# Kernel optimization log

Hardware: AMD Instinct MI355X
Metric: run time of the kernel (lower is better)

## Reference

```python
import jax, jax.numpy as jnp
import numpy as np

B, NA, NE = 1024, 15, 16
N_AGENTS = NA + 1
BN = B * N_AGENTS
D_OWN = D_ALL = D_EN = 32
H, NH, NMOVE, RD = 256, 4, 6, 8
HD = H // NH
GATE = 1.0
NEG = -1e9  # stand-in for -inf (safe under autodiff)


def _gelu(x):
    return jax.nn.gelu(x, approximate=False)  # torch nn.GELU default is exact


def _ln(x, g, b, eps=1e-5):
    m = x.mean(-1, keepdims=True)
    v = ((x - m) ** 2).mean(-1, keepdims=True)
    return (x - m) * jax.lax.rsqrt(v + eps) * g + b


def _masked_mean(x, mask, axis):
    w = mask[..., None].astype(x.dtype)
    return (x * w).sum(axis) / jnp.clip(w.sum(axis), 1e-8)


def _mha(q, kv, mask, Wq, Wk, Wv, Wo):
    # q: [BN,H], kv: [BN,M,H], mask: [BN,M] bool
    bn = q.shape[0]
    qh = (q @ Wq.T).reshape(bn, NH, HD)
    kh = (kv @ Wk.T).reshape(bn, -1, NH, HD)
    vh = (kv @ Wv.T).reshape(bn, -1, NH, HD)
    scores = jnp.einsum('bhd,bmhd->bhm', qh, kh) / np.sqrt(HD)
    scores = jnp.where(mask[:, None, :], scores, NEG)
    attn = jax.nn.softmax(scores, axis=-1)
    ctx = jnp.einsum('bhm,bmhd->bhd', attn, vh).reshape(bn, H)
    return ctx @ Wo.T


def setup_inputs() -> dict:
    key = jax.random.key(0)
    ks = iter(jax.random.split(key, 64))
    nrm = lambda *s: jax.random.normal(next(ks), s, dtype=jnp.float32)
    w = lambda o, i: nrm(o, i) * 0.02
    inp = dict(
        bs=B,
        own_feats=nrm(BN, 1, D_OWN),
        ally_feats=nrm(BN, NA, D_ALL),
        enemy_feats=nrm(BN, NE, D_EN),
        hidden_state=nrm(B, N_AGENTS, H),
        own_W=w(H, D_OWN), own_b=jnp.zeros(H),
        ally_W=w(H, D_ALL), ally_b=jnp.zeros(H),
        en_W=w(H, D_EN), en_b=jnp.zeros(H),
        aA_Wq=w(H, H), aA_Wk=w(H, H), aA_Wv=w(H, H), aA_Wo=w(H, H),
        aE_Wq=w(H, H), aE_Wk=w(H, H), aE_Wv=w(H, H), aE_Wo=w(H, H),
        fuse_W1=w(H, 3 * H), fuse_b1=jnp.zeros(H), fuse_g1=jnp.ones(H), fuse_be1=jnp.zeros(H),
        fuse_W2=w(H, H), fuse_b2=jnp.zeros(H),
        pool_W1=w(128, 3 * H), pool_b1=jnp.zeros(128), pool_g1=jnp.ones(128), pool_be1=jnp.zeros(128),
        pool_W2=w(128, 128), pool_b2=jnp.zeros(128),
        role_W1=w(128, 128), role_b1=jnp.zeros(128), role_g1=jnp.ones(128), role_be1=jnp.zeros(128),
        role_W2=w(RD, 128), role_b2=jnp.zeros(RD),
        rln_g=jnp.ones(RD), rln_b=jnp.zeros(RD),
        gru_Wih=w(3 * H, H + RD), gru_Whh=w(3 * H, H),
        gru_bih=jnp.zeros(3 * H), gru_bhh=jnp.zeros(3 * H),
        qn_W=w(NMOVE, H), qn_b=jnp.zeros(NMOVE),
        qp_W=w(H, H + RD), kp_W=w(H, H),
    )
    return inp


def reference(bs, own_feats, ally_feats, enemy_feats, hidden_state,
              own_W, own_b, ally_W, ally_b, en_W, en_b,
              aA_Wq, aA_Wk, aA_Wv, aA_Wo, aE_Wq, aE_Wk, aE_Wv, aE_Wo,
              fuse_W1, fuse_b1, fuse_g1, fuse_be1, fuse_W2, fuse_b2,
              pool_W1, pool_b1, pool_g1, pool_be1, pool_W2, pool_b2,
              role_W1, role_b1, role_g1, role_be1, role_W2, role_b2,
              rln_g, rln_b, gru_Wih, gru_Whh, gru_bih, gru_bhh,
              qn_W, qn_b, qp_W, kp_W):
    ally_mask = ~jnp.all(ally_feats == 0, axis=-1)   # [BN,Na]
    enemy_mask = ~jnp.all(enemy_feats == 0, axis=-1)  # [BN,Ne]

    own_e = own_feats @ own_W.T + own_b        # [BN,1,H]
    ally_e = ally_feats @ ally_W.T + ally_b    # [BN,Na,H]
    enemy_e = enemy_feats @ en_W.T + en_b      # [BN,Ne,H]
    self_emb = own_e[:, 0]                     # [BN,H]

    cA = _mha(self_emb, ally_e, ally_mask, aA_Wq, aA_Wk, aA_Wv, aA_Wo)
    cE = _mha(self_emb, enemy_e, enemy_mask, aE_Wq, aE_Wk, aE_Wv, aE_Wo)

    # fuse MLP: Linear -> GELU -> LN -> Linear
    f_in = jnp.concatenate([self_emb, cA, cE], axis=-1)
    h0 = _ln(_gelu(f_in @ fuse_W1.T + fuse_b1), fuse_g1, fuse_be1) @ fuse_W2.T + fuse_b2

    pA = _masked_mean(ally_e, ally_mask, 1)
    pE = _masked_mean(enemy_e, enemy_mask, 1)
    p_in = jnp.concatenate([self_emb, pA, pE], axis=-1)
    pooled = _ln(_gelu(p_in @ pool_W1.T + pool_b1), pool_g1, pool_be1) @ pool_W2.T + pool_b2
    r = jnp.tanh(_ln(_gelu(pooled @ role_W1.T + role_b1), role_g1, role_be1) @ role_W2.T + role_b2)
    r = _ln(r, rln_g, rln_b)

    # GRUCell (torch convention)
    h_prev = hidden_state.reshape(-1, H)
    x = jnp.concatenate([h0, GATE * r], axis=-1)
    gi = x @ gru_Wih.T + gru_bih
    gh = h_prev @ gru_Whh.T + gru_bhh
    i_r, i_z, i_n = jnp.split(gi, 3, axis=-1)
    h_r, h_z, h_n = jnp.split(gh, 3, axis=-1)
    rg = jax.nn.sigmoid(i_r + h_r)
    zg = jax.nn.sigmoid(i_z + h_z)
    ng = jnp.tanh(i_n + rg * h_n)
    h_cur = (1.0 - zg) * ng + zg * h_prev

    q_normal = h_cur @ qn_W.T + qn_b  # [BN,n_move]

    q_vec = jnp.concatenate([h_cur, GATE * r], axis=-1) @ qp_W.T  # [BN,H]
    k_vec = enemy_e @ kp_W.T                                       # [BN,Ne,H]
    logits = jnp.einsum('bj,bmj->bm', q_vec, k_vec) / np.sqrt(H)
    logits = jnp.where(enemy_mask, logits, NEG)
    denom = jnp.clip(enemy_mask.sum(-1, keepdims=True), 1).astype(logits.dtype)
    mean_valid = jnp.where(enemy_mask, logits, 0.0).sum(-1, keepdims=True) / denom
    q_interact = logits - mean_valid

    Q = jnp.concatenate([q_normal, q_interact], axis=-1)
    h_out = h_cur.reshape(bs, N_AGENTS, H)
    return Q, h_out
```

## Files before the change

### kernel.cpp

```cpp
#include <hip/hip_runtime.h>
#include <hip/hip_bf16.h>


#define MROWS 16384

typedef __attribute__((ext_vector_type(8))) short short8;
typedef __attribute__((ext_vector_type(4))) float float4v;
typedef __attribute__((ext_vector_type(4))) unsigned short ushort4v;
typedef __attribute__((ext_vector_type(2))) unsigned short ushort2v;

__device__ __forceinline__ unsigned short f2b(float f) {
    __hip_bfloat16 h = __float2bfloat16(f);
    return *reinterpret_cast<unsigned short*>(&h);
}
__device__ __forceinline__ float b2f(unsigned short u) {
    __hip_bfloat16 h;
    *reinterpret_cast<unsigned short*>(&h) = u;
    return __bfloat162float(h);
}
__device__ __forceinline__ void gll16(const unsigned short* g, unsigned short* l) {
    __builtin_amdgcn_global_load_lds((const __attribute__((address_space(1))) void*)g,
                                     (__attribute__((address_space(3))) void*)l, 16, 0, 0);
}

__global__ void cvt_misc(const float* __restrict__ hidden, const float* __restrict__ ownf,
                         unsigned short* __restrict__ XG, unsigned short* __restrict__ OWNb,
                         unsigned short* __restrict__ zbuf) {
    int idx = blockIdx.x * 256 + threadIdx.x;
    const int nh = MROWS * 64;
    const int no = MROWS * 8;
    if (idx < nh) {
        int row = idx >> 6, c4 = (idx & 63) * 4;
        float4 v = *(const float4*)(hidden + (size_t)row * 256 + c4);
        ushort4v d = { f2b(v.x), f2b(v.y), f2b(v.z), f2b(v.w) };
        *(ushort4v*)(XG + (size_t)row * 520 + 264 + c4) = d;
    } else if (idx < nh + no) {
        int j = idx - nh;
        int row = j >> 3, c4 = (j & 7) * 4;
        float4 v = *(const float4*)(ownf + (size_t)row * 32 + c4);
        ushort4v d = { f2b(v.x), f2b(v.y), f2b(v.z), f2b(v.w) };
        *(ushort4v*)(OWNb + (size_t)row * 32 + c4) = d;
    } else if (idx < nh + no + 16) {
        int j = idx - nh - no;
        ((uint4*)zbuf)[j] = make_uint4(0u, 0u, 0u, 0u);
    }
}

struct TOp {
    int type;
    const float* A; int sAi, sAk;
    const float* B; int sBj, sBk;
    void* O; int sOi;
    int I, J, K;
    int nb; int aB, bB, oB;
};
struct TOpSet { int n; int tiles[26]; TOp ops[26]; };

__global__ __launch_bounds__(256)
void compose_tiled(TOpSet S) {
    int t = blockIdx.x;
    int op = 0;
    while (op < S.n && t >= S.tiles[op]) { t -= S.tiles[op]; op++; }
    if (op >= S.n) return;
    TOp o = S.ops[op];
    int ti = (o.I + 31) >> 5, tj = (o.J + 31) >> 5;
    int per = ti * tj;
    int b = t / per;
    int rem = t - b * per;
    int i0 = (rem / tj) * 32, j0 = (rem % tj) * 32;
    int tid = threadIdx.x;
    if (o.type >= 2) {
        for (int e = tid; e < 1024; e += 256) {
            int r = e >> 5, c = e & 31;
            int i = i0 + r, j = j0 + c;
            if (i < o.I && j < o.J) {
                unsigned short v = 0;
                if (o.type == 2) v = f2b(o.A[(long)b * o.aB + (long)i * o.sAi + (long)j * o.sAk]);
                ((unsigned short*)o.O)[(long)b * o.oB + (long)i * o.sOi + j] = v;
            }
        }
        return;
    }
    __shared__ float As[32][33];
    __shared__ float Bs[32][33];
    int tx = tid & 15, ty = tid >> 4;
    float a00 = 0.f, a01 = 0.f, a10 = 0.f, a11 = 0.f;
    const float* Ab = o.A + (long)b * o.aB;
    const float* Bb = o.B + (long)b * o.bB;
    for (int k0 = 0; k0 < o.K; k0 += 32) {
        for (int e = tid; e < 1024; e += 256) {
            int r = e >> 5, c = e & 31;
            As[r][c] = (i0 + r < o.I && k0 + c < o.K)
                       ? Ab[(long)(i0 + r) * o.sAi + (long)(k0 + c) * o.sAk] : 0.f;
            Bs[r][c] = (k0 + r < o.K && j0 + c < o.J)
                       ? Bb[(long)(j0 + c) * o.sBj + (long)(k0 + r) * o.sBk] : 0.f;
        }
        __syncthreads();
#pragma unroll
        for (int k = 0; k < 32; k++) {
            float x0 = As[ty * 2][k], x1 = As[ty * 2 + 1][k];
            float y0 = Bs[k][tx * 2], y1 = Bs[k][tx * 2 + 1];
            a00 += x0 * y0; a01 += x0 * y1; a10 += x1 * y0; a11 += x1 * y1;
        }
        __syncthreads();
    }
    int i = i0 + ty * 2, j = j0 + tx * 2;
    float vals[2][2] = {{a00, a01}, {a10, a11}};
#pragma unroll
    for (int di = 0; di < 2; di++)
#pragma unroll
        for (int dj = 0; dj < 2; dj++) {
            int ii = i + di, jj = j + dj;
            if (ii < o.I && jj < o.J) {
                long oidx = (long)b * o.oB + (long)ii * o.sOi + jj;
                if (o.type == 0) ((unsigned short*)o.O)[oidx] = f2b(vals[di][dj]);
                else ((float*)o.O)[oidx] = vals[di][dj];
            }
        }
}

struct MOp { const float* A; int sAi; const float* x; const float* b1; const float* b2; float* out; int I, K; };
struct MOpSet { int n; int waves[10]; MOp ops[10]; };

__global__ void mv_ops(MOpSet S) {
    int wid = blockIdx.x * 4 + (threadIdx.x >> 6);
    int lane = threadIdx.x & 63;
    int op = 0;
    while (op < S.n && wid >= S.waves[op]) { wid -= S.waves[op]; op++; }
    if (op >= S.n) return;
    MOp o = S.ops[op];
    float s = 0.f;
    for (int k = lane; k < o.K; k += 64) s += o.A[(long)wid * o.sAi + k] * o.x[k];
    for (int off = 32; off; off >>= 1) s += __shfl_xor(s, off, 64);
    if (lane == 0) {
        if (o.b1) s += o.b1[wid];
        if (o.b2) s += o.b2[wid];
        o.out[wid] = s;
    }
}

template<int BM, int BN>
__global__ __launch_bounds__(256, 4)
void gemm_bf16(const unsigned short* __restrict__ A, int lda,
               const unsigned short* __restrict__ W,
               const float* __restrict__ bias,
               unsigned short* __restrict__ C, int ldc,
               int N, int K, int act,
               const unsigned short* __restrict__ zbuf) {
    constexpr int MI = BM / 32, NJ = BN / 32;
    __shared__ __align__(16) unsigned short As[2][BM * 32];
    __shared__ __align__(16) unsigned short Bs[2][BN * 32];
    int tid = threadIdx.x;
    int m0 = blockIdx.x * BM, n0 = blockIdx.y * BN;
    int wave = tid >> 6, lane = tid & 63;
    int wm = (wave & 1) * (BM / 2), wn = (wave >> 1) * (BN / 2);
    int l16 = lane & 15, quad = lane >> 4;

    float4v acc[MI][NJ];
#pragma unroll
    for (int i = 0; i < MI; i++)
#pragma unroll
        for (int j = 0; j < NJ; j++) acc[i][j] = (float4v){0.f, 0.f, 0.f, 0.f};

    int swz = ((l16 >> 1) & 3) * 8;
    int nt = (K + 31) >> 5;

    auto stage = [&](int buf, int k0) {
#pragma unroll
        for (int s0 = 0; s0 < BM * 4; s0 += 256) {
            int s = s0 + tid;
            int row = s >> 2;
            int cg = (s & 3) ^ ((row >> 1) & 3);
            int ka = k0 + cg * 8;
            gll16((ka < K) ? A + (size_t)(m0 + row) * lda + ka : zbuf, &As[buf][s * 8]);
        }
#pragma unroll
        for (int s0 = 0; s0 < BN * 4; s0 += 256) {
            int s = s0 + tid;
            int row = s >> 2;
            int cg = (s & 3) ^ ((row >> 1) & 3);
            int ka = k0 + cg * 8;
            gll16((ka < K && n0 + row < N) ? W + (size_t)(n0 + row) * K + ka : zbuf,
                  &Bs[buf][s * 8]);
        }
    };
    auto compute = [&](int buf) {
        short8 a[MI], b[NJ];
#pragma unroll
        for (int i = 0; i < MI; i++)
            a[i] = *(const short8*)(&As[buf][(wm + i * 16 + l16) * 32 + ((quad * 8) ^ swz)]);
#pragma unroll
        for (int j = 0; j < NJ; j++)
            b[j] = *(const short8*)(&Bs[buf][(wn + j * 16 + l16) * 32 + ((quad * 8) ^ swz)]);
#pragma unroll
        for (int i = 0; i < MI; i++)
#pragma unroll
            for (int j = 0; j < NJ; j++)
                acc[i][j] = __builtin_amdgcn_mfma_f32_16x16x32_bf16(a[i], b[j], acc[i][j], 0, 0, 0);
    };

    stage(0, 0);
    asm volatile("s_waitcnt vmcnt(0)" ::: "memory");
    __builtin_amdgcn_s_barrier();
    for (int t = 0; t < nt - 1; t++) {
        stage((t + 1) & 1, (t + 1) << 5);
        compute(t & 1);
        asm volatile("s_waitcnt vmcnt(0)" ::: "memory");
        __builtin_amdgcn_s_barrier();
    }
    compute((nt - 1) & 1);

#pragma unroll
    for (int i = 0; i < MI; i++) {
#pragma unroll
        for (int j = 0; j < NJ; j++) {
#pragma unroll
            for (int rr = 0; rr < 4; rr++) {
                int rowm = m0 + wm + i * 16 + quad * 4 + rr;
                int coln = wn + j * 16 + l16;
                if (n0 + coln >= N) continue;
                float v = acc[i][j][rr];
                if (bias) v += bias[n0 + coln];
                if (act == 1) v = 0.5f * v * (1.f + erff(v * 0.70710678f));
                C[(size_t)rowm * ldc + n0 + coln] = f2b(v);
            }
        }
    }
}

__global__ __launch_bounds__(256)
void ln_fp(const unsigned short* __restrict__ FPC,
           const float* __restrict__ g1, const float* __restrict__ be1,
           const float* __restrict__ g2, const float* __restrict__ be2,
           unsigned short* __restrict__ XG, unsigned short* __restrict__ T2) {
    int tid = threadIdx.x;
    size_t row = (size_t)blockIdx.x * 4 + (tid >> 6);
    int l = tid & 63;
    const unsigned short* src = FPC + row * 384;
    ushort4v vf = *(const ushort4v*)(src + l * 4);
    ushort2v vp = *(const ushort2v*)(src + 256 + l * 2);
    float f0 = b2f(vf[0]), f1 = b2f(vf[1]), f2v = b2f(vf[2]), f3 = b2f(vf[3]);
    float p0 = b2f(vp[0]), p1 = b2f(vp[1]);
    float s = f0 + f1 + f2v + f3;
    float q = f0 * f0 + f1 * f1 + f2v * f2v + f3 * f3;
    float s2 = p0 + p1, q2 = p0 * p0 + p1 * p1;
    for (int o = 32; o; o >>= 1) {
        s += __shfl_xor(s, o, 64); q += __shfl_xor(q, o, 64);
        s2 += __shfl_xor(s2, o, 64); q2 += __shfl_xor(q2, o, 64);
    }
    float mean = s * (1.f / 256.f);
    float rstd = rsqrtf(q * (1.f / 256.f) - mean * mean + 1e-5f);
    float4 g = *(const float4*)(g1 + l * 4);
    float4 be = *(const float4*)(be1 + l * 4);
    ushort4v o4;
    o4[0] = f2b((f0 - mean) * rstd * g.x + be.x);
    o4[1] = f2b((f1 - mean) * rstd * g.y + be.y);
    o4[2] = f2b((f2v - mean) * rstd * g.z + be.z);
    o4[3] = f2b((f3 - mean) * rstd * g.w + be.w);
    *(ushort4v*)(XG + row * 520 + l * 4) = o4;
    float mean2 = s2 * (1.f / 128.f);
    float rstd2 = rsqrtf(q2 * (1.f / 128.f) - mean2 * mean2 + 1e-5f);
    float2 gg = *(const float2*)(g2 + l * 2);
    float2 bb = *(const float2*)(be2 + l * 2);
    ushort2v o2;
    o2[0] = f2b((p0 - mean2) * rstd2 * gg.x + bb.x);
    o2[1] = f2b((p1 - mean2) * rstd2 * gg.y + bb.y);
    *(ushort2v*)(T2 + row * 128 + l * 2) = o2;
}

__global__ __launch_bounds__(256)
void glue_attn(const float* __restrict__ allyf, const float* __restrict__ enemyf,
               const float* __restrict__ ownf, const unsigned short* __restrict__ QKS,
               unsigned short* __restrict__ X) {
    __shared__ __align__(16) float af[4][540];
    __shared__ __align__(16) float ef[4][576];
    __shared__ __align__(16) float qk[4][288];
    __shared__ float attnA[4][64];
    __shared__ float attnE[4][64];
    __shared__ float mskA[4][16];
    __shared__ float mskE[4][16];
    int tid = threadIdx.x;
    size_t rb = (size_t)blockIdx.x * 4;

    for (int idx = tid; idx < 480; idx += 256) {
        int r = idx / 120, ch = idx - r * 120;
        float4 v = *(const float4*)(allyf + ((rb + r) * 480 + ch * 4));
        *(float4*)&af[r][(ch >> 3) * 36 + (ch & 7) * 4] = v;
    }
    for (int idx = tid; idx < 512; idx += 256) {
        int r = idx >> 7, ch = idx & 127;
        float4 v = *(const float4*)(enemyf + ((rb + r) * 512 + ch * 4));
        *(float4*)&ef[r][(ch >> 3) * 36 + (ch & 7) * 4] = v;
    }
    if (tid < 128) {
        int r = tid >> 5, ch = tid & 31;
        short8 v = *(const short8*)(QKS + (rb + r) * 256 + ch * 8);
#pragma unroll
        for (int j = 0; j < 8; j++)
            qk[r][(ch >> 2) * 36 + (ch & 3) * 8 + j] = b2f((unsigned short)v[j]);
    } else {
        int r = (tid - 128) >> 5, c = (tid - 128) & 31;
        X[(rb + r) * 360 + c] = f2b(ownf[(rb + r) * 32 + c]);
    }
    if (tid < 24) {
        int r = tid / 6, c = 98 + tid % 6;
        X[(rb + r) * 360 + c] = 0;
    }
    __syncthreads();

    if (tid < 248) {
        int pair = tid >> 1, half = tid & 1;
        int r = pair / 31, e = pair - r * 31;
        const float* base = (e < 15) ? &af[r][e * 36] : &ef[r][(e - 15) * 36];
        const float4* b4 = (const float4*)base + half * 4;
        bool nz = false;
#pragma unroll
        for (int k = 0; k < 4; k++) {
            float4 v = b4[k];
            nz |= (v.x != 0.f) || (v.y != 0.f) || (v.z != 0.f) || (v.w != 0.f);
        }
        int other = __shfl_xor((int)nz, 1, 64);
        float mv = (nz || other != 0) ? 1.f : 0.f;
        if (half == 0) {
            if (e < 15) mskA[r][e] = mv; else mskE[r][e - 15] = mv;
        }
    } else if (tid < 252) {
        mskA[tid - 248][15] = 0.f;
    }
    __syncthreads();

    int r = tid >> 6, lane = tid & 63;
    int h = lane >> 4, m = lane & 15;
    {
        float sc = -3.0e38f;
        if (m < 15) {
            const float4* qa = (const float4*)&qk[r][h * 36];
            const float4* aa = (const float4*)&af[r][m * 36];
            float s = 0.f;
#pragma unroll
            for (int k = 0; k < 8; k++) {
                float4 q = qa[k], a = aa[k];
                s += q.x * a.x + q.y * a.y + q.z * a.z + q.w * a.w;
            }
            sc = (mskA[r][m] > 0.f) ? s * 0.125f : -1e9f;
        }
        float mx = sc;
        for (int o = 8; o; o >>= 1) mx = fmaxf(mx, __shfl_xor(mx, o, 64));
        float e = (m < 15) ? __expf(sc - mx) : 0.f;
        float sm = e;
        for (int o = 8; o; o >>= 1) sm += __shfl_xor(sm, o, 64);
        attnA[r][h * 16 + m] = e / sm;
    }
    {
        const float4* qa = (const float4*)&qk[r][(4 + h) * 36];
        const float4* aa = (const float4*)&ef[r][m * 36];
        float s = 0.f;
#pragma unroll
        for (int k = 0; k < 8; k++) {
            float4 q = qa[k], a = aa[k];
            s += q.x * a.x + q.y * a.y + q.z * a.z + q.w * a.w;
        }
        float sc = (mskE[r][m] > 0.f) ? s * 0.125f : -1e9f;
        float mx = sc;
        for (int o = 8; o; o >>= 1) mx = fmaxf(mx, __shfl_xor(mx, o, 64));
        float e = __expf(sc - mx);
        float sm = e;
        for (int o = 8; o; o >>= 1) sm += __shfl_xor(sm, o, 64);
        attnE[r][h * 16 + m] = e / sm;
    }
    __syncthreads();
    size_t row = rb + r;
#pragma unroll
    for (int it = 0; it < 2; it++) {
        int idx = lane + it * 64;
        int hh = idx >> 5, c = idx & 31;
        float sA = 0.f;
        for (int mm = 0; mm < 15; mm++) sA += attnA[r][hh * 16 + mm] * af[r][mm * 36 + c];
        X[row * 360 + 104 + idx] = f2b(sA);
        float sE = 0.f;
        for (int mm = 0; mm < 16; mm++) sE += attnE[r][hh * 16 + mm] * ef[r][mm * 36 + c];
        X[row * 360 + 232 + idx] = f2b(sE);
    }
    if (lane < 32) {
        float cnt = 0.f;
        for (int mm = 0; mm < 15; mm++) cnt += mskA[r][mm];
        float s = 0.f;
        for (int mm = 0; mm < 15; mm++) s += af[r][mm * 36 + lane];
        X[row * 360 + 32 + lane] = f2b(s / fmaxf(cnt, 1e-8f));
        if (lane == 0) X[row * 360 + 96] = f2b(cnt > 0.f ? 1.f : 0.f);
    } else {
        int c = lane - 32;
        float cnt = 0.f;
        for (int mm = 0; mm < 16; mm++) cnt += mskE[r][mm];
        float s = 0.f;
        for (int mm = 0; mm < 16; mm++) s += ef[r][mm * 36 + c];
        X[row * 360 + 64 + c] = f2b(s / fmaxf(cnt, 1e-8f));
        if (c == 0) X[row * 360 + 97] = f2b(cnt > 0.f ? 1.f : 0.f);
    }
}

__global__ __launch_bounds__(256)
void ln_role(const unsigned short* __restrict__ T3, const float* __restrict__ g1,
             const float* __restrict__ be1, const float* __restrict__ W2,
             const float* __restrict__ b2, const float* __restrict__ rg,
             const float* __restrict__ rb, unsigned short* __restrict__ XG) {
    __shared__ float t3[32][132];
    __shared__ float gl[128], bl[128];
    int tid = threadIdx.x;
    size_t base = (size_t)blockIdx.x * 4096;
    for (int idx = tid; idx < 4096; idx += 256)
        t3[idx >> 7][idx & 127] = b2f(T3[base + idx]);
    if (tid < 128) { gl[tid] = g1[tid]; bl[tid] = be1[tid]; }
    __syncthreads();
    int r = tid >> 3, t = tid & 7;
    float s = 0.f, q = 0.f;
    for (int c = 0; c < 16; c++) { float v = t3[r][t * 16 + c]; s += v; q += v * v; }
    for (int o = 4; o; o >>= 1) { s += __shfl_xor(s, o, 8); q += __shfl_xor(q, o, 8); }
    float mean = s * (1.f / 128.f);
    float var = q * (1.f / 128.f) - mean * mean;
    float rstd = rsqrtf(var + 1e-5f);
    float acc = b2[t];
    const float* w = W2 + t * 128;
    for (int d = 0; d < 128; d++)
        acc += w[d] * ((t3[r][d] - mean) * rstd * gl[d] + bl[d]);
    float v = tanhf(acc);
    float mn = v;
    for (int o = 4; o; o >>= 1) mn += __shfl_xor(mn, o, 8);
    mn *= 0.125f;
    float dv = v - mn, qq = dv * dv;
    for (int o = 4; o; o >>= 1) qq += __shfl_xor(qq, o, 8);
    qq *= 0.125f;
    size_t row = (size_t)blockIdx.x * 32 + r;
    XG[row * 520 + 256 + t] = f2b(dv * rsqrtf(qq + 1e-5f) * rg[t] + rb[t]);
}

__global__ __launch_bounds__(256)
void glue_gru(const unsigned short* __restrict__ G, const float* __restrict__ hp,
              float* __restrict__ hout, unsigned short* __restrict__ XQ,
              const unsigned short* __restrict__ XG) {
    int tid = threadIdx.x;
    size_t row = (size_t)blockIdx.x * 4 + (tid >> 6);
    int l = tid & 63;
    size_t b = row * 1024;
    ushort4v vr = *(const ushort4v*)(G + b + l * 4);
    ushort4v vz = *(const ushort4v*)(G + b + 256 + l * 4);
    ushort4v vi = *(const ushort4v*)(G + b + 512 + l * 4);
    ushort4v vh = *(const ushort4v*)(G + b + 768 + l * 4);
    float4 hv = *(const float4*)(hp + row * 256 + l * 4);
    float hpv[4] = {hv.x, hv.y, hv.z, hv.w};
    float hov[4];
    ushort4v xq;
#pragma unroll
    for (int j = 0; j < 4; j++) {
        float rg = 1.f / (1.f + __expf(-b2f(vr[j])));
        float zg = 1.f / (1.f + __expf(-b2f(vz[j])));
        float ng = tanhf(b2f(vi[j]) + rg * b2f(vh[j]));
        float h = (1.f - zg) * ng + zg * hpv[j];
        hov[j] = h;
        xq[j] = f2b(h);
    }
    *(float4*)(hout + row * 256 + l * 4) = make_float4(hov[0], hov[1], hov[2], hov[3]);
    *(ushort4v*)(XQ + row * 264 + l * 4) = xq;
    if (l < 2)
        ((ushort4v*)(XQ + row * 264 + 256))[l] = ((const ushort4v*)(XG + row * 520 + 256))[l];
}

__global__ __launch_bounds__(256)
void glue_final(const unsigned short* __restrict__ QWS, const float* __restrict__ efeats,
                const float* __restrict__ qnb, float* __restrict__ Q) {
    __shared__ __align__(16) float ef[8][576];
    __shared__ __align__(16) float qw[8][40];
    int tid = threadIdx.x;
    size_t rb = (size_t)blockIdx.x * 8;
    for (int idx = tid; idx < 1024; idx += 256) {
        int r = idx >> 7, ch = idx & 127;
        float4 v = *(const float4*)(efeats + (rb + r) * 512 + ch * 4);
        *(float4*)&ef[r][(ch >> 3) * 36 + (ch & 7) * 4] = v;
    }
    for (int idx = tid; idx < 320; idx += 256) {
        int r = idx / 40, c = idx % 40;
        qw[r][c] = b2f(QWS[(rb + r) * 40 + c]);
    }
    __syncthreads();
    int r = tid >> 5, t = tid & 31;
    size_t row = rb + r;
    float lg = 0.f, mk = 0.f;
    if (t < 16) {
        const float4* fr = (const float4*)&ef[r][t * 36];
        const float4* qv = (const float4*)&qw[r][0];
        bool nz = false;
        float s = 0.f;
#pragma unroll
        for (int k = 0; k < 8; k++) {
            float4 a = fr[k], b = qv[k];
            nz |= (a.x != 0.f) || (a.y != 0.f) || (a.z != 0.f) || (a.w != 0.f);
            s += a.x * b.x + a.y * b.y + a.z * b.z + a.w * b.w;
        }
        mk = nz ? 1.f : 0.f;
        lg = (s + qw[r][32]) * 0.0625f;
    }
    float sv = mk * lg, cv = mk;
    for (int o = 8; o; o >>= 1) { sv += __shfl_xor(sv, o, 64); cv += __shfl_xor(cv, o, 64); }
    float mean = sv / fmaxf(cv, 1.f);
    if (t < 16) Q[row * 22 + 6 + t] = (mk > 0.f ? lg : -1e9f) - mean;
    if (t < 6) Q[row * 22 + t] = qw[r][33 + t] + qnb[t];
}

extern "C" void kernel_launch(void* const* d_in, const int* in_sizes, int n_in,
                              void* d_out, int out_size, void* d_ws, size_t ws_size,
                              hipStream_t stream) {
    const float* own_feats = (const float*)d_in[1];
    const float* ally_feats = (const float*)d_in[2];
    const float* enemy_feats = (const float*)d_in[3];
    const float* hidden = (const float*)d_in[4];
    const float* own_W = (const float*)d_in[5];   const float* own_b = (const float*)d_in[6];
    const float* ally_W = (const float*)d_in[7];  const float* ally_b = (const float*)d_in[8];
    const float* en_W = (const float*)d_in[9];    const float* en_b = (const float*)d_in[10];
    const float* aA_Wq = (const float*)d_in[11];  const float* aA_Wk = (const float*)d_in[12];
    const float* aA_Wv = (const float*)d_in[13];  const float* aA_Wo = (const float*)d_in[14];
    const float* aE_Wq = (const float*)d_in[15];  const float* aE_Wk = (const float*)d_in[16];
    const float* aE_Wv = (const float*)d_in[17];  const float* aE_Wo = (const float*)d_in[18];
    const float* fuse_W1 = (const float*)d_in[19]; const float* fuse_b1 = (const float*)d_in[20];
    const float* fuse_g1 = (const float*)d_in[21]; const float* fuse_be1 = (const float*)d_in[22];
    const float* fuse_W2 = (const float*)d_in[23]; const float* fuse_b2 = (const float*)d_in[24];
    const float* pool_W1 = (const float*)d_in[25]; const float* pool_b1 = (const float*)d_in[26];
    const float* pool_g1 = (const float*)d_in[27]; const float* pool_be1 = (const float*)d_in[28];
    const float* pool_W2 = (const float*)d_in[29]; const float* pool_b2 = (const float*)d_in[30];
    const float* role_W1 = (const float*)d_in[31]; const float* role_b1 = (const float*)d_in[32];
    const float* role_g1 = (const float*)d_in[33]; const float* role_be1 = (const float*)d_in[34];
    const float* role_W2 = (const float*)d_in[35]; const float* role_b2 = (const float*)d_in[36];
    const float* rln_g = (const float*)d_in[37];   const float* rln_b = (const float*)d_in[38];
    const float* gru_Wih = (const float*)d_in[39]; const float* gru_Whh = (const float*)d_in[40];
    const float* gru_bih = (const float*)d_in[41]; const float* gru_bhh = (const float*)d_in[42];
    const float* qn_W = (const float*)d_in[43];    const float* qn_b = (const float*)d_in[44];
    const float* qp_W = (const float*)d_in[45];    const float* kp_W = (const float*)d_in[46];

    char* wsp = (char*)d_ws;
    size_t off = 0;
    auto alloc = [&](size_t bytes) { void* p = wsp + off; off = (off + bytes + 255) & ~(size_t)255; return p; };

    unsigned short* X    = (unsigned short*)alloc((size_t)MROWS * 360 * 2);
    unsigned short* XG   = (unsigned short*)alloc((size_t)MROWS * 520 * 2);
    unsigned short* FPC  = (unsigned short*)alloc((size_t)MROWS * 384 * 2);
    unsigned short* GIb  = (unsigned short*)alloc((size_t)MROWS * 1024 * 2);
    unsigned short* XQ   = (unsigned short*)alloc((size_t)MROWS * 264 * 2);
    unsigned short* T2b  = (unsigned short*)alloc((size_t)MROWS * 128 * 2);
    unsigned short* T3b  = (unsigned short*)alloc((size_t)MROWS * 128 * 2);
    unsigned short* QKSb = (unsigned short*)alloc((size_t)MROWS * 256 * 2);
    unsigned short* QWSb = (unsigned short*)alloc((size_t)MROWS * 40 * 2);
    unsigned short* OWNb = (unsigned short*)alloc((size_t)MROWS * 32 * 2);
    unsigned short* FPW  = (unsigned short*)alloc(384 * 360 * 2);
    unsigned short* WGRU = (unsigned short*)alloc(1024 * 520 * 2);
    unsigned short* QWSW = (unsigned short*)alloc(40 * 264 * 2);
    unsigned short* WQKSO= (unsigned short*)alloc(256 * 32 * 2);
    unsigned short* rpW  = (unsigned short*)alloc(128 * 128 * 2);
    unsigned short* zbuf = (unsigned short*)alloc(256);
    float* WkAp = (float*)alloc(256 * 32 * 4);
    float* WvAp = (float*)alloc(256 * 32 * 4);
    float* WkEp = (float*)alloc(256 * 32 * 4);
    float* WvEp = (float*)alloc(256 * 32 * 4);
    float* Wkpp = (float*)alloc(256 * 32 * 4);
    float* WQKS_AE = (float*)alloc(256 * 256 * 4);
    float* WoVA = (float*)alloc(256 * 128 * 4);
    float* WoVE = (float*)alloc(256 * 128 * 4);
    float* bvAp = (float*)alloc(256 * 4);
    float* bvEp = (float*)alloc(256 * 4);
    float* bkpp = (float*)alloc(256 * 4);
    float* vall = (float*)alloc(768 * 4);
    float* qksb = (float*)alloc(256 * 4);
    float* fpb  = (float*)alloc(384 * 4);
    float* gbias= (float*)alloc(1024 * 4);
    float* rpb  = (float*)alloc(128 * 4);

    float* Qout = (float*)d_out;
    float* Hout = Qout + (size_t)MROWS * 22;

    auto tilesOf = [](const TOp& o) {
        return o.nb * (((o.I + 31) / 32) * ((o.J + 31) / 32));
    };

    cvt_misc<<<(MROWS * 64 + MROWS * 8 + 16 + 255) / 256, 256, 0, stream>>>(hidden, own_feats, XG, OWNb, zbuf);

    {
        MOpSet S; S.n = 5; int waves = 0;
        S.ops[0] = {aA_Wv, 256, ally_b, nullptr, nullptr, bvAp, 256, 256};
        S.ops[1] = {aE_Wv, 256, en_b, nullptr, nullptr, bvEp, 256, 256};
        S.ops[2] = {kp_W, 256, en_b, nullptr, nullptr, bkpp, 256, 256};
        S.ops[3] = {nullptr, 0, nullptr, own_b, nullptr, vall, 256, 0};
        S.ops[4] = {role_W1, 128, pool_b2, role_b1, nullptr, rpb, 128, 128};
        for (int i = 0; i < S.n; i++) { S.waves[i] = S.ops[i].I; waves += S.ops[i].I; }
        mv_ops<<<(waves + 3) / 4, 256, 0, stream>>>(S);
    }
    {
        TOpSet S; S.n = 0; int grid = 0;
        auto add = [&](TOp o) { S.tiles[S.n] = tilesOf(o); grid += S.tiles[S.n]; S.ops[S.n++] = o; };
        add({1, aA_Wk, 256, 1, ally_W, 1, 32, WkAp, 32, 256, 32, 256, 1, 0, 0, 0});
        add({1, aA_Wv, 256, 1, ally_W, 1, 32, WvAp, 32, 256, 32, 256, 1, 0, 0, 0});
        add({1, aE_Wk, 256, 1, en_W, 1, 32, WkEp, 32, 256, 32, 256, 1, 0, 0, 0});
        add({1, aE_Wv, 256, 1, en_W, 1, 32, WvEp, 32, 256, 32, 256, 1, 0, 0, 0});
        add({1, kp_W, 256, 1, en_W, 1, 32, Wkpp, 32, 256, 32, 256, 1, 0, 0, 0});
        compose_tiled<<<grid, 256, 0, stream>>>(S);
    }
    {
        TOpSet S; S.n = 0; int grid = 0;
        auto add = [&](TOp o) { S.tiles[S.n] = tilesOf(o); grid += S.tiles[S.n]; S.ops[S.n++] = o; };
        add({1, WkAp, 1, 32, aA_Wq, 1, 256, WQKS_AE, 256, 32, 256, 64, 4, 2048, 16384, 8192});
        add({1, WkEp, 1, 32, aE_Wq, 1, 256, WQKS_AE + 128 * 256, 256, 32, 256, 64, 4, 2048, 16384, 8192});
        add({1, aA_Wo, 256, 1, WvAp, 1, 32, WoVA, 128, 256, 32, 64, 4, 64, 2048, 32});
        add({1, aE_Wo, 256, 1, WvEp, 1, 32, WoVE, 128, 256, 32, 64, 4, 64, 2048, 32});
        compose_tiled<<<grid, 256, 0, stream>>>(S);
    }
    {
        MOpSet S; S.n = 3; int waves = 0;
        S.ops[0] = {aA_Wo, 256, bvAp, nullptr, nullptr, vall + 256, 256, 256};
        S.ops[1] = {aE_Wo, 256, bvEp, nullptr, nullptr, vall + 512, 256, 256};
        S.ops[2] = {WQKS_AE, 256, own_b, nullptr, nullptr, qksb, 256, 256};
        for (int i = 0; i < S.n; i++) { S.waves[i] = S.ops[i].I; waves += S.ops[i].I; }
        mv_ops<<<(waves + 3) / 4, 256, 0, stream>>>(S);
    }
    {
        MOpSet S; S.n = 5; int waves = 0;
        S.ops[0] = {fuse_W1, 768, vall, fuse_b1, nullptr, fpb, 256, 768};
        S.ops[1] = {pool_W1, 768, vall, pool_b1, nullptr, fpb + 256, 128, 256};
        S.ops[2] = {gru_Wih, 264, fuse_b2, gru_bih, gru_bhh, gbias, 512, 256};
        S.ops[3] = {gru_Wih + 512 * 264, 264, fuse_b2, gru_bih + 512, nullptr, gbias + 512, 256, 256};
        S.ops[4] = {nullptr, 0, nullptr, gru_bhh + 512, nullptr, gbias + 768, 256, 0};
        for (int i = 0; i < S.n; i++) { S.waves[i] = S.ops[i].I; waves += S.ops[i].I; }
        mv_ops<<<(waves + 3) / 4, 256, 0, stream>>>(S);
    }
    {
        TOpSet S; S.n = 0; int grid = 0;
        auto add = [&](TOp o) { S.tiles[S.n] = tilesOf(o); grid += S.tiles[S.n]; S.ops[S.n++] = o; };
        add({0, fuse_W1, 768, 1, own_W, 1, 32, FPW, 360, 256, 32, 256, 1, 0, 0, 0});
        add({3, nullptr, 0, 0, nullptr, 0, 0, FPW + 32, 360, 256, 72, 0, 1, 0, 0, 0});
        add({0, fuse_W1 + 256, 768, 1, WoVA, 1, 128, FPW + 104, 360, 256, 128, 256, 1, 0, 0, 0});
        add({0, fuse_W1 + 512, 768, 1, WoVE, 1, 128, FPW + 232, 360, 256, 128, 256, 1, 0, 0, 0});
        add({0, pool_W1, 768, 1, own_W, 1, 32, FPW + 256 * 360, 360, 128, 32, 256, 1, 0, 0, 0});
        add({0, pool_W1 + 256, 768, 1, ally_W, 1, 32, FPW + 256 * 360 + 32, 360, 128, 32, 256, 1, 0, 0, 0});
        add({0, pool_W1 + 512, 768, 1, en_W, 1, 32, FPW + 256 * 360 + 64, 360, 128, 32, 256, 1, 0, 0, 0});
        add({0, pool_W1 + 256, 768, 1, ally_b, 0, 1, FPW + 256 * 360 + 96, 360, 128, 1, 256, 1, 0, 0, 0});
        add({0, pool_W1 + 512, 768, 1, en_b, 0, 1, FPW + 256 * 360 + 97, 360, 128, 1, 256, 1, 0, 0, 0});
        add({3, nullptr, 0, 0, nullptr, 0, 0, FPW + 256 * 360 + 98, 360, 128, 262, 0, 1, 0, 0, 0});
        add({0, gru_Wih, 264, 1, fuse_W2, 1, 256, WGRU, 520, 512, 256, 256, 1, 0, 0, 0});
        add({2, gru_Wih + 256, 264, 1, nullptr, 0, 0, WGRU + 256, 520, 512, 8, 0, 1, 0, 0, 0});
        add({2, gru_Whh, 256, 1, nullptr, 0, 0, WGRU + 264, 520, 512, 256, 0, 1, 0, 0, 0});
        add({0, gru_Wih + 512 * 264, 264, 1, fuse_W2, 1, 256, WGRU + 512 * 520, 520, 256, 256, 256, 1, 0, 0, 0});
        add({2, gru_Wih + 512 * 264 + 256, 264, 1, nullptr, 0, 0, WGRU + 512 * 520 + 256, 520, 256, 8, 0, 1, 0, 0, 0});
        add({3, nullptr, 0, 0, nullptr, 0, 0, WGRU + 512 * 520 + 264, 520, 256, 256, 0, 1, 0, 0, 0});
        add({3, nullptr, 0, 0, nullptr, 0, 0, WGRU + 768 * 520, 520, 256, 264, 0, 1, 0, 0, 0});
        add({2, gru_Whh + 512 * 256, 256, 1, nullptr, 0, 0, WGRU + 768 * 520 + 264, 520, 256, 256, 0, 1, 0, 0, 0});
        add({0, Wkpp, 1, 32, qp_W, 1, 264, QWSW, 264, 32, 264, 256, 1, 0, 0, 0});
        add({0, bkpp, 0, 1, qp_W, 1, 264, QWSW + 32 * 264, 264, 1, 264, 256, 1, 0, 0, 0});
        add({2, qn_W, 256, 1, nullptr, 0, 0, QWSW + 33 * 264, 264, 6, 256, 0, 1, 0, 0, 0});
        add({3, nullptr, 0, 0, nullptr, 0, 0, QWSW + 33 * 264 + 256, 264, 6, 8, 0, 1, 0, 0, 0});
        add({3, nullptr, 0, 0, nullptr, 0, 0, QWSW + 39 * 264, 264, 1, 264, 0, 1, 0, 0, 0});
        add({0, WQKS_AE, 256, 1, own_W, 1, 32, WQKSO, 32, 256, 32, 256, 1, 0, 0, 0});
        add({0, role_W1, 128, 1, pool_W2, 1, 128, rpW, 128, 128, 128, 128, 1, 0, 0, 0});
        compose_tiled<<<grid, 256, 0, stream>>>(S);
    }

    auto gemm = [&](const unsigned short* A, int lda, const unsigned short* Wm, const float* bias,
                    unsigned short* C, int ldc, int N, int K, int act) {
        gemm_bf16<64, 64><<<dim3(MROWS / 64, (N + 63) / 64), 256, 0, stream>>>(
            A, lda, Wm, bias, C, ldc, N, K, act, zbuf);
    };

    gemm(OWNb, 32, WQKSO, qksb, QKSb, 256, 256, 32, 0);
    glue_attn<<<MROWS / 4, 256, 0, stream>>>(ally_feats, enemy_feats, own_feats, QKSb, X);
    gemm(X, 360, FPW, fpb, FPC, 384, 384, 360, 1);
    ln_fp<<<MROWS / 4, 256, 0, stream>>>(FPC, fuse_g1, fuse_be1, pool_g1, pool_be1, XG, T2b);
    gemm(T2b, 128, rpW, rpb, T3b, 128, 128, 128, 1);
    ln_role<<<MROWS / 32, 256, 0, stream>>>(T3b, role_g1, role_be1, role_W2, role_b2, rln_g, rln_b, XG);
    gemm(XG, 520, WGRU, gbias, GIb, 1024, 1024, 520, 0);
    glue_gru<<<MROWS / 4, 256, 0, stream>>>(GIb, hidden, Hout, XQ, XG);
    gemm(XQ, 264, QWSW, nullptr, QWSb, 40, 40, 264, 0);
    glue_final<<<MROWS / 8, 256, 0, stream>>>(QWSb, enemy_feats, qn_b, Qout);
}
```

Before: 435.0 us.

## Fuse GRU gate GEMM with GRU cell epilogue in one kernel

After: 413.8 us, median of 2. -4.9%, faster.

```diff
diff --git a/kernel.cpp b/kernel.cpp
--- a/kernel.cpp
+++ b/kernel.cpp
@@ -228,6 +228,100 @@
     }
 }
 
+__global__ __launch_bounds__(256, 4)
+void gemm_gru(const unsigned short* __restrict__ A, int lda,
+              const unsigned short* __restrict__ W,
+              const float* __restrict__ gbias,
+              const float* __restrict__ hp,
+              float* __restrict__ hout, unsigned short* __restrict__ XQ,
+              int K, const unsigned short* __restrict__ zbuf) {
+    __shared__ __align__(16) unsigned short As[2][64 * 32];
+    __shared__ __align__(16) unsigned short Ws[2][4 * 64 * 32];
+    int tid = threadIdx.x;
+    int m0 = blockIdx.x * 64, n0 = blockIdx.y * 64;
+    int wave = tid >> 6, lane = tid & 63;
+    int wm = (wave & 1) * 32, wn = (wave >> 1) * 32;
+    int l16 = lane & 15, quad = lane >> 4;
+
+    float4v acc[4][2][2];
+#pragma unroll
+    for (int g = 0; g < 4; g++)
+#pragma unroll
+        for (int i = 0; i < 2; i++)
+#pragma unroll
+            for (int j = 0; j < 2; j++) acc[g][i][j] = (float4v){0.f, 0.f, 0.f, 0.f};
+
+    int swz = ((l16 >> 1) & 3) * 8;
+    int nt = (K + 31) >> 5;
+    int srow = tid >> 2;
+    int cg = (tid & 3) ^ ((srow >> 1) & 3);
+    const unsigned short* Arow = A + (size_t)(m0 + srow) * lda + cg * 8;
+    const unsigned short* Wrow[4];
+#pragma unroll
+    for (int g = 0; g < 4; g++)
+        Wrow[g] = W + (size_t)(g * 256 + n0 + srow) * K + cg * 8;
+    int kaOff = cg * 8;
+
+    auto stage = [&](int buf, int k0) {
+        int ka = k0 + kaOff;
+        gll16((ka < K) ? Arow + k0 : zbuf, &As[buf][tid * 8]);
+#pragma unroll
+        for (int g = 0; g < 4; g++)
+            gll16((ka < K) ? Wrow[g] + k0 : zbuf, &Ws[buf][(g * 256 + tid) * 8]);
+    };
+    auto compute = [&](int buf) {
+        short8 a[2], b[4][2];
+#pragma unroll
+        for (int i = 0; i < 2; i++)
+            a[i] = *(const short8*)(&As[buf][(wm + i * 16 + l16) * 32 + ((quad * 8) ^ swz)]);
+#pragma unroll
+        for (int g = 0; g < 4; g++)
+#pragma unroll
+            for (int j = 0; j < 2; j++)
+                b[g][j] = *(const short8*)(&Ws[buf][g * 2048 + (wn + j * 16 + l16) * 32 + ((quad * 8) ^ swz)]);
+#pragma unroll
+        for (int g = 0; g < 4; g++)
+#pragma unroll
+            for (int i = 0; i < 2; i++)
+#pragma unroll
+                for (int j = 0; j < 2; j++)
+                    acc[g][i][j] = __builtin_amdgcn_mfma_f32_16x16x32_bf16(a[i], b[g][j], acc[g][i][j], 0, 0, 0);
+    };
+
+    stage(0, 0);
+    asm volatile("s_waitcnt vmcnt(0)" ::: "memory");
+    __builtin_amdgcn_s_barrier();
+    for (int t = 0; t < nt - 1; t++) {
+        stage((t + 1) & 1, (t + 1) << 5);
+        compute(t & 1);
+        asm volatile("s_waitcnt vmcnt(0)" ::: "memory");
+        __builtin_amdgcn_s_barrier();
+    }
+    compute((nt - 1) & 1);
+
+#pragma unroll
+    for (int i = 0; i < 2; i++) {
+#pragma unroll
+        for (int j = 0; j < 2; j++) {
+#pragma unroll
+            for (int rr = 0; rr < 4; rr++) {
+                int rowm = m0 + wm + i * 16 + quad * 4 + rr;
+                int coln = n0 + wn + j * 16 + l16;
+                float r_ = acc[0][i][j][rr] + gbias[coln];
+                float z_ = acc[1][i][j][rr] + gbias[256 + coln];
+                float in_ = acc[2][i][j][rr] + gbias[512 + coln];
+                float hn_ = acc[3][i][j][rr] + gbias[768 + coln];
+                float rg = 1.f / (1.f + __expf(-r_));
+                float zg = 1.f / (1.f + __expf(-z_));
+                float ng = tanhf(in_ + rg * hn_);
+                float h = (1.f - zg) * ng + zg * hp[(size_t)rowm * 256 + coln];
+                hout[(size_t)rowm * 256 + coln] = h;
+                XQ[(size_t)rowm * 264 + coln] = f2b(h);
+            }
+        }
+    }
+}
+
 __global__ __launch_bounds__(256)
 void ln_fp(const unsigned short* __restrict__ FPC,
            const float* __restrict__ g1, const float* __restrict__ be1,
@@ -403,7 +497,8 @@
 void ln_role(const unsigned short* __restrict__ T3, const float* __restrict__ g1,
              const float* __restrict__ be1, const float* __restrict__ W2,
              const float* __restrict__ b2, const float* __restrict__ rg,
-             const float* __restrict__ rb, unsigned short* __restrict__ XG) {
+             const float* __restrict__ rb, unsigned short* __restrict__ XG,
+             unsigned short* __restrict__ XQ) {
     __shared__ float t3[32][132];
     __shared__ float gl[128], bl[128];
     int tid = threadIdx.x;
@@ -431,38 +526,9 @@
     for (int o = 4; o; o >>= 1) qq += __shfl_xor(qq, o, 8);
     qq *= 0.125f;
     size_t row = (size_t)blockIdx.x * 32 + r;
-    XG[row * 520 + 256 + t] = f2b(dv * rsqrtf(qq + 1e-5f) * rg[t] + rb[t]);
-}
-
-__global__ __launch_bounds__(256)
-void glue_gru(const unsigned short* __restrict__ G, const float* __restrict__ hp,
-              float* __restrict__ hout, unsigned short* __restrict__ XQ,
-              const unsigned short* __restrict__ XG) {
-    int tid = threadIdx.x;
-    size_t row = (size_t)blockIdx.x * 4 + (tid >> 6);
-    int l = tid & 63;
-    size_t b = row * 1024;
-    ushort4v vr = *(const ushort4v*)(G + b + l * 4);
-    ushort4v vz = *(const ushort4v*)(G + b + 256 + l * 4);
-    ushort4v vi = *(const ushort4v*)(G + b + 512 + l * 4);
-    ushort4v vh = *(const ushort4v*)(G + b + 768 + l * 4);
-    float4 hv = *(const float4*)(hp + row * 256 + l * 4);
-    float hpv[4] = {hv.x, hv.y, hv.z, hv.w};
-    float hov[4];
-    ushort4v xq;
-#pragma unroll
-    for (int j = 0; j < 4; j++) {
-        float rg = 1.f / (1.f + __expf(-b2f(vr[j])));
-        float zg = 1.f / (1.f + __expf(-b2f(vz[j])));
-        float ng = tanhf(b2f(vi[j]) + rg * b2f(vh[j]));
-        float h = (1.f - zg) * ng + zg * hpv[j];
-        hov[j] = h;
-        xq[j] = f2b(h);
-    }
-    *(float4*)(hout + row * 256 + l * 4) = make_float4(hov[0], hov[1], hov[2], hov[3]);
-    *(ushort4v*)(XQ + row * 264 + l * 4) = xq;
-    if (l < 2)
-        ((ushort4v*)(XQ + row * 264 + 256))[l] = ((const ushort4v*)(XG + row * 520 + 256))[l];
+    unsigned short ov = f2b(dv * rsqrtf(qq + 1e-5f) * rg[t] + rb[t]);
+    XG[row * 520 + 256 + t] = ov;
+    XQ[row * 264 + 256 + t] = ov;
 }
 
 __global__ __launch_bounds__(256)
@@ -542,7 +608,6 @@
     unsigned short* X    = (unsigned short*)alloc((size_t)MROWS * 360 * 2);
     unsigned short* XG   = (unsigned short*)alloc((size_t)MROWS * 520 * 2);
     unsigned short* FPC  = (unsigned short*)alloc((size_t)MROWS * 384 * 2);
-    unsigned short* GIb  = (unsigned short*)alloc((size_t)MROWS * 1024 * 2);
     unsigned short* XQ   = (unsigned short*)alloc((size_t)MROWS * 264 * 2);
     unsigned short* T2b  = (unsigned short*)alloc((size_t)MROWS * 128 * 2);
     unsigned short* T3b  = (unsigned short*)alloc((size_t)MROWS * 128 * 2);
@@ -670,9 +735,9 @@
     gemm(X, 360, FPW, fpb, FPC, 384, 384, 360, 1);
     ln_fp<<<MROWS / 4, 256, 0, stream>>>(FPC, fuse_g1, fuse_be1, pool_g1, pool_be1, XG, T2b);
     gemm(T2b, 128, rpW, rpb, T3b, 128, 128, 128, 1);
-    ln_role<<<MROWS / 32, 256, 0, stream>>>(T3b, role_g1, role_be1, role_W2, role_b2, rln_g, rln_b, XG);
-    gemm(XG, 520, WGRU, gbias, GIb, 1024, 1024, 520, 0);
-    glue_gru<<<MROWS / 4, 256, 0, stream>>>(GIb, hidden, Hout, XQ, XG);
+    ln_role<<<MROWS / 32, 256, 0, stream>>>(T3b, role_g1, role_be1, role_W2, role_b2, rln_g, rln_b, XG, XQ);
+    gemm_gru<<<dim3(MROWS / 64, 4), 256, 0, stream>>>(XG, 520, WGRU, gbias, hidden,
+                                                      Hout, XQ, 520, zbuf);
     gemm(XQ, 264, QWSW, nullptr, QWSb, 40, 40, 264, 0);
     glue_final<<<MROWS / 8, 256, 0, stream>>>(QWSb, enemy_feats, qn_b, Qout);
 }
```
